# Performance work log

Measured on AMD Instinct MI355X. Metric: run time of the kernel, lower is better.

The kernel has to match this reference:

```python
import jax, jax.numpy as jnp
import numpy as np

N, C, T, V = 16, 128, 150, 25
NH, DK, DV = 8, 32, 128          # dk = 0.25*128, dv = out_channels
DKH, DVH = DK // NH, DV // NH    # 4, 16
EPS = 1e-5


def setup_inputs() -> dict:
    key = jax.random.key(0)
    ks = jax.random.split(key, 14)
    qkv_out = 2 * DK + DV  # 192
    return {
        "x": jax.random.normal(ks[0], (N, C, T, V), jnp.float32),
        "qkv_w": jax.random.normal(ks[1], (qkv_out, C), jnp.float32) * (1.0 / np.sqrt(C)),
        "qkv_b": jax.random.normal(ks[2], (qkv_out,), jnp.float32) * 0.01,
        "key_rel": jax.random.normal(ks[3], (2 * T - 1, DKH), jnp.float32),
        "attn_w": jax.random.normal(ks[4], (DV, DV), jnp.float32) * (1.0 / np.sqrt(DV)),
        "attn_b": jax.random.normal(ks[5], (DV,), jnp.float32) * 0.01,
        "dbn_g": jnp.ones((C * V,), jnp.float32),
        "dbn_b": jnp.zeros((C * V,), jnp.float32),
        "dbn_m": jax.random.normal(ks[6], (C * V,), jnp.float32) * 0.01,
        "dbn_v": jax.random.uniform(ks[7], (C * V,), jnp.float32, 0.5, 1.5),
        "bn_g": jnp.ones((DV,), jnp.float32),
        "bn_b": jnp.zeros((DV,), jnp.float32),
        "bn_m": jax.random.normal(ks[8], (DV,), jnp.float32) * 0.01,
        "bn_v": jax.random.uniform(ks[9], (DV,), jnp.float32, 0.5, 1.5),
    }


def rel_to_abs(x):
    # x: [B, H, L, 2L-1] relative logits -> [B, H, L, L] absolute logits
    B, H, L, _ = x.shape
    x = jnp.pad(x, ((0, 0), (0, 0), (0, 0), (0, 1)))          # [B,H,L,2L]
    flat = x.reshape(B, H, L * 2 * L)
    flat = jnp.pad(flat, ((0, 0), (0, 0), (0, L - 1)))
    return flat.reshape(B, H, L + 1, 2 * L - 1)[:, :, :L, L - 1:]


def reference(x, qkv_w, qkv_b, key_rel, attn_w, attn_b,
              dbn_g, dbn_b, dbn_m, dbn_v, bn_g, bn_b, bn_m, bn_v):
    n, c, t, v = x.shape
    x_sum = x
    # data_bn (BatchNorm1d over C*V channels, inference mode)
    xn = x.transpose(0, 1, 3, 2).reshape(n, c * v, t)
    xn = (xn - dbn_m[None, :, None]) * (dbn_g / jnp.sqrt(dbn_v + EPS))[None, :, None] + dbn_b[None, :, None]
    xn = xn.reshape(n, c, v, t).transpose(0, 1, 3, 2)
    # fold nodes into batch: [N,C,T,V] -> [N*V, C, T]
    xb = xn.transpose(0, 3, 1, 2).reshape(n * v, c, t)
    # pointwise qkv conv (kernel 1x1)
    qkv = jnp.einsum('bct,oc->bot', xb, qkv_w) + qkv_b[None, :, None]
    q = qkv[:, :DK]
    k = qkv[:, DK:2 * DK]
    val = qkv[:, 2 * DK:]
    B = n * v
    q = q.reshape(B, NH, DKH, t) * (DKH ** -0.5)   # scaled before rel logits, as in torch
    k = k.reshape(B, NH, DKH, t)
    val = val.reshape(B, NH, DVH, t)
    logits = jnp.einsum('bhdt,bhds->bhts', q, k)    # [B,NH,T,T]
    rel = jnp.einsum('bhdt,md->bhtm', q, key_rel)   # [B,NH,T,2T-1]
    logits = logits + rel_to_abs(rel)
    weights = jax.nn.softmax(logits, axis=-1)
    out = jnp.einsum('bhts,bhds->bhtd', weights, val)  # [B,NH,T,DVH]
    # combine heads -> [B, DV, T], then 1x1 attn_out conv
    out = out.transpose(0, 1, 3, 2).reshape(B, DV, t)
    out = jnp.einsum('bct,oc->bot', out, attn_w) + attn_b[None, :, None]
    # unfold nodes: [N*V, DV, T] -> [N, DV, T, V]
    out = out.reshape(n, v, DV, t).transpose(0, 2, 3, 1)
    res = out + x_sum
    # BatchNorm2d over channel dim (inference mode)
    res = (res - bn_m[None, :, None, None]) * (bn_g / jnp.sqrt(bn_v + EPS))[None, :, None, None] + bn_b[None, :, None, None]
    return jax.nn.relu(res)
```

## Files before the change

### kernel.cpp

```cpp
#include <hip/hip_runtime.h>
#include <math.h>

#define N_   16
#define C_   128
#define T_   150
#define V_   25
#define NH_  8
#define DK_  32
#define DV_  128
#define B_   400
#define QO_  192
#define EPS_ 1e-5f

typedef __attribute__((ext_vector_type(4))) short bf16x4;
typedef __attribute__((ext_vector_type(4))) float f32x4;
typedef __attribute__((ext_vector_type(8))) short short8;

__device__ inline f32x4 mfma16(bf16x4 a, bf16x4 b, f32x4 c) {
#if __has_builtin(__builtin_amdgcn_mfma_f32_16x16x16bf16_1k)
  return __builtin_amdgcn_mfma_f32_16x16x16bf16_1k(a, b, c, 0, 0, 0);
#else
  asm volatile("v_mfma_f32_16x16x16_bf16 %0, %1, %2, %0"
               : "+v"(c) : "v"(a), "v"(b));
  return c;
#endif
}

__device__ inline short f2bf(float f) {
  union { float f; unsigned u; } v; v.f = f;
  unsigned u = v.u + 0x7fffu + ((v.u >> 16) & 1u);
  return (short)(u >> 16);
}
__device__ inline float lo16(unsigned u) { union { unsigned u; float f; } v; v.u = u << 16;        return v.f; }
__device__ inline float hi16(unsigned u) { union { unsigned u; float f; } v; v.u = u & 0xffff0000u; return v.f; }
__device__ inline unsigned pk2(float a, float b) {
  union { float f; unsigned u; } x, y; x.f = a; y.f = b;
  return ((x.u + 0x8000u) >> 16) | ((y.u + 0x8000u) & 0xffff0000u);
}
__device__ inline unsigned pktr(float a, float b) {
  union { float f; unsigned u; } x, y; x.f = a; y.f = b;
#if __has_builtin(__builtin_amdgcn_perm)
  return __builtin_amdgcn_perm(y.u, x.u, 0x07060302u);
#else
  return (x.u >> 16) | (y.u & 0xffff0000u);
#endif
}

__global__ __launch_bounds__(256) void k_prep(
    const float* __restrict__ qkv_w, const float* __restrict__ attn_w,
    const float* __restrict__ dbn_g, const float* __restrict__ dbn_b,
    const float* __restrict__ dbn_m, const float* __restrict__ dbn_v,
    const float* __restrict__ key_rel,
    short* __restrict__ wqb, short* __restrict__ wab,
    short* __restrict__ krbg,
    float* __restrict__ dsc, float* __restrict__ dsh)
{
  const int tid = blockIdx.x*256 + threadIdx.x;
  const int nthr = gridDim.x*256;
  for (int i = tid; i < QO_*C_; i += nthr) wqb[i] = f2bf(qkv_w[i]);
  for (int i = tid; i < DV_*DV_; i += nthr) wab[i] = f2bf(attn_w[i]);
  for (int i = tid; i < 336*4; i += nthr) {
    int m = (i >> 2) - 16;
    krbg[i] = (m >= 0 && m < 2*T_-1) ? f2bf(key_rel[m*4 + (i & 3)]) : (short)0;
  }
  for (int i = tid; i < C_*V_; i += nthr) {
    float sc = dbn_g[i] * rsqrtf(dbn_v[i] + EPS_);
    dsc[i] = sc;
    dsh[i] = dbn_b[i] - dbn_m[i]*sc;
  }
}

__global__ __launch_bounds__(256) void k_xt2(
    const float* __restrict__ x, const float* __restrict__ dsc,
    const float* __restrict__ dsh, short* __restrict__ xtb)
{
  const int n = blockIdx.x, tv0 = blockIdx.y * 125;
  __shared__ short ls[C_][126];
  for (int i = threadIdx.x; i < C_*125; i += 256) {
    int c = i / 125, j = i % 125;
    int cv = c*V_ + j % 25;
    ls[c][j] = f2bf(x[((size_t)n*C_ + c)*(T_*V_) + tv0 + j] * dsc[cv] + dsh[cv]);
  }
  __syncthreads();
  for (int i = threadIdx.x; i < 125*C_; i += 256) {
    int j = i >> 7, c = i & 127;
    int tv = tv0 + j, t = tv / 25, v = tv % 25;
    xtb[((size_t)(n*V_ + v)*T_ + t)*C_ + c] = ls[c][j];
  }
}

__global__ __launch_bounds__(256) void k_qkv(
    const short* __restrict__ xtb, const short* __restrict__ wqb,
    const float* __restrict__ qkv_b, short* __restrict__ qkvb)
{
  const int b = blockIdx.x, t0 = blockIdx.y * 80;
  __shared__ short xs[80][136];
  for (int i = threadIdx.x; i < 80*16; i += 256) {
    int tt = i >> 4, ch = i & 15, t = t0 + tt;
    short8 vv = {0,0,0,0,0,0,0,0};
    if (t < T_) vv = *(const short8*)&xtb[((size_t)b*T_ + t)*C_ + ch*8];
    *(short8*)&xs[tt][ch*8] = vv;
  }
  __syncthreads();
  const int wave = threadIdx.x >> 6, lane = threadIdx.x & 63;
  const int tl = lane & 15, g = lane >> 4;
  const int ob = wave * 48;

  bf16x4 afr[3][8];
  #pragma unroll
  for (int mt = 0; mt < 3; ++mt)
    #pragma unroll
    for (int ks = 0; ks < 8; ++ks)
      afr[mt][ks] = *(const bf16x4*)&wqb[(ob + mt*16 + tl)*C_ + ks*16 + g*4];

  const f32x4 zero = {0.f,0.f,0.f,0.f};
  f32x4 acc[3][5];
  #pragma unroll
  for (int mt = 0; mt < 3; ++mt)
    #pragma unroll
    for (int nt = 0; nt < 5; ++nt) acc[mt][nt] = zero;

  #pragma unroll
  for (int ks = 0; ks < 8; ++ks) {
    bf16x4 bfr[5];
    #pragma unroll
    for (int nt = 0; nt < 5; ++nt)
      bfr[nt] = *(const bf16x4*)&xs[nt*16 + tl][ks*16 + g*4];
    #pragma unroll
    for (int mt = 0; mt < 3; ++mt)
      #pragma unroll
      for (int nt = 0; nt < 5; ++nt)
        acc[mt][nt] = mfma16(afr[mt][ks], bfr[nt], acc[mt][nt]);
  }

  float bia[3][4], scm[3];
  #pragma unroll
  for (int mt = 0; mt < 3; ++mt) {
    scm[mt] = (ob + mt*16 < DK_) ? (0.5f*1.44269504f) : 1.f;
    #pragma unroll
    for (int r = 0; r < 4; ++r) bia[mt][r] = qkv_b[ob + mt*16 + g*4 + r];
  }

  #pragma unroll
  for (int nt = 0; nt < 5; ++nt) {
    int tg = t0 + nt*16 + tl;
    if (tg >= T_) continue;
    #pragma unroll
    for (int mt = 0; mt < 3; ++mt) {
      int o = ob + mt*16 + g*4;
      short* dst = &qkvb[((size_t)b*QO_ + o)*T_ + tg];
      #pragma unroll
      for (int r = 0; r < 4; ++r)
        dst[r*T_] = f2bf((acc[mt][nt][r] + bia[mt][r]) * scm[mt]);
    }
  }
}

__global__ __launch_bounds__(256) void k_attn(
    const short* __restrict__ qkvb, const short* __restrict__ krbg,
    short* __restrict__ o2b)
{
  const int bh = blockIdx.x;
  const int b  = bh >> 3, h = bh & 7;
  __shared__ short kbc[160*4];
  __shared__ short qbc[160*4];
  __shared__ short ve[16][164];
  __shared__ short krb[336*4];
  const short* base = qkvb + (size_t)b*QO_*T_;
  const int tid = threadIdx.x;

  for (int i = tid; i < 320; i += 256) {
    int d = i / 80, j = i % 80, s = 2*j;
    unsigned u = 0;
    if (j < 75) u = *(const unsigned*)&base[(DK_ + h*4 + d)*T_ + s];
    kbc[s*4 + d] = (short)u;
    kbc[(s+1)*4 + d] = (short)(u >> 16);
  }
  for (int i = tid; i < 320; i += 256) {
    int d = i / 80, j = i % 80, t = 2*j;
    unsigned u = 0;
    if (j < 75) u = *(const unsigned*)&base[(h*4 + d)*T_ + t];
    qbc[t*4 + d] = (short)u;
    qbc[(t+1)*4 + d] = (short)(u >> 16);
  }
  for (int i = tid; i < 1280; i += 256) {
    int e = i / 80, j = i % 80;
    unsigned u = 0;
    if (j < 75) u = *(const unsigned*)&base[(2*DK_ + h*16 + e)*T_ + 2*j];
    *(unsigned*)&ve[e][2*j] = u;
  }
  for (int i = tid; i < 672; i += 256)
    *(unsigned*)&krb[2*i] = *(const unsigned*)&krbg[2*i];
  __syncthreads();

  const int wave = tid >> 6, lane = tid & 63;
  const int tl = lane & 15, g = lane >> 4, soff = g << 2;

  const bf16x4 zerob = {0, 0, 0, 0};
  const f32x4 zero = {0.f, 0.f, 0.f, 0.f};

  bf16x4 kfr[10], vfr[10];
  #pragma unroll
  for (int st = 0; st < 10; ++st) {
    kfr[st] = (g == 0) ? *(const bf16x4*)&kbc[(st*16 + tl)*4] : zerob;
    vfr[st] = *(const bf16x4*)&ve[tl][st*16 + soff];
  }

  const bool act = (g == (tl & 3));
  const int kca = tl >> 2;

  for (int tt = wave; tt < 10; tt += 4) {
    const int t0 = tt*16, tg = t0 + tl;
    union { unsigned u[2]; bf16x4 v; } bqu;
    bqu.v = *(const bf16x4*)&qbc[tg*4];
    const bf16x4 qfr = (g == 0) ? bqu.v : zerob;

    f32x4 c[10];
    #pragma unroll
    for (int st = 0; st < 10; ++st) c[st] = mfma16(kfr[st], qfr, zero);

    bf16x4 brel[4];
    #pragma unroll
    for (int kc = 0; kc < 4; ++kc)
      brel[kc] = (act && kc == kca) ? bqu.v : zerob;

    const bf16x4* krp = ((const bf16x4*)krb) + (tl - g + 165 - t0);
    #pragma unroll
    for (int st = 0; st < 10; ++st)
      #pragma unroll
      for (int kc = 0; kc < 4; ++kc)
        c[st] = mfma16(krp[st*16 - kc*4], brel[kc], c[st]);

    #pragma unroll
    for (int i = 0; i < 4; ++i)
      if (soff + i >= 6) c[9][i] = -3.0e38f;

    float l = 0.f;
    f32x4 acc = zero;
    #pragma unroll
    for (int st = 0; st < 10; ++st) {
      float p0 = __builtin_exp2f(c[st][0]);
      float p1 = __builtin_exp2f(c[st][1]);
      float p2 = __builtin_exp2f(c[st][2]);
      float p3 = __builtin_exp2f(c[st][3]);
      l += (p0 + p1) + (p2 + p3);
      union { unsigned u[2]; bf16x4 v; } pf;
      pf.u[0] = pktr(p0, p1); pf.u[1] = pktr(p2, p3);
      acc = mfma16(vfr[st], pf.v, acc);
    }
    l += __shfl_xor(l, 16);
    l += __shfl_xor(l, 32);
    const float inv = __builtin_amdgcn_rcpf(l);

    if (tg < T_) {
      unsigned u0 = pk2(acc[0]*inv, acc[1]*inv);
      unsigned u1 = pk2(acc[2]*inv, acc[3]*inv);
      *(uint2*)&o2b[((size_t)b*T_ + tg)*DV_ + h*16 + soff] = make_uint2(u0, u1);
    }
  }
}

__global__ __launch_bounds__(256) void k_proj(
    const short* __restrict__ o2b, const short* __restrict__ wab,
    const float* __restrict__ attn_b, short* __restrict__ projb)
{
  const int b = blockIdx.x, t0 = blockIdx.y * 80;
  __shared__ short xs[80][136];
  for (int i = threadIdx.x; i < 80*16; i += 256) {
    int tt = i >> 4, ch = i & 15, t = t0 + tt;
    short8 vv = {0,0,0,0,0,0,0,0};
    if (t < T_) vv = *(const short8*)&o2b[((size_t)b*T_ + t)*DV_ + ch*8];
    *(short8*)&xs[tt][ch*8] = vv;
  }
  __syncthreads();
  const int wave = threadIdx.x >> 6, lane = threadIdx.x & 63;
  const int tl = lane & 15, g = lane >> 4;
  const int ob = wave * 32;

  bf16x4 afr[2][8];
  #pragma unroll
  for (int mt = 0; mt < 2; ++mt)
    #pragma unroll
    for (int ks = 0; ks < 8; ++ks)
      afr[mt][ks] = *(const bf16x4*)&wab[(ob + mt*16 + tl)*DV_ + ks*16 + g*4];

  const f32x4 zero = {0.f,0.f,0.f,0.f};
  f32x4 acc[2][5];
  #pragma unroll
  for (int mt = 0; mt < 2; ++mt)
    #pragma unroll
    for (int nt = 0; nt < 5; ++nt) acc[mt][nt] = zero;

  #pragma unroll
  for (int ks = 0; ks < 8; ++ks) {
    bf16x4 bfr[5];
    #pragma unroll
    for (int nt = 0; nt < 5; ++nt)
      bfr[nt] = *(const bf16x4*)&xs[nt*16 + tl][ks*16 + g*4];
    #pragma unroll
    for (int mt = 0; mt < 2; ++mt)
      #pragma unroll
      for (int nt = 0; nt < 5; ++nt)
        acc[mt][nt] = mfma16(afr[mt][ks], bfr[nt], acc[mt][nt]);
  }

  float bia[2][4];
  #pragma unroll
  for (int mt = 0; mt < 2; ++mt)
    #pragma unroll
    for (int r = 0; r < 4; ++r) bia[mt][r] = attn_b[ob + mt*16 + g*4 + r];

  #pragma unroll
  for (int nt = 0; nt < 5; ++nt) {
    int tg = t0 + nt*16 + tl;
    if (tg >= T_) continue;
    #pragma unroll
    for (int mt = 0; mt < 2; ++mt) {
      int o = ob + mt*16 + g*4;
      short* dst = &projb[((size_t)b*DV_ + o)*T_ + tg];
      #pragma unroll
      for (int r = 0; r < 4; ++r)
        dst[r*T_] = f2bf(acc[mt][nt][r] + bia[mt][r]);
    }
  }
}

__global__ __launch_bounds__(256) void k_final(
    const short* __restrict__ projb, const float* __restrict__ x,
    const float* __restrict__ bn_g, const float* __restrict__ bn_b,
    const float* __restrict__ bn_m, const float* __restrict__ bn_v,
    float* __restrict__ out)
{
  const int n = blockIdx.x, o = blockIdx.y;
  __shared__ short ls[V_*T_];
  for (int i = threadIdx.x; i < V_*T_; i += 256) {
    int v = i / T_, t = i % T_;
    ls[i] = projb[((size_t)(n*V_ + v)*DV_ + o)*T_ + t];
  }
  __syncthreads();
  const float sc = bn_g[o] * rsqrtf(bn_v[o] + EPS_);
  const float sh = bn_b[o] - bn_m[o]*sc;
  const size_t base = ((size_t)n*C_ + o)*(T_*V_);
  for (int j = threadIdx.x; j < T_*V_; j += 256) {
    int t = j / V_, v = j % V_;
    float pv = lo16((unsigned)(unsigned short)ls[v*T_ + t]);
    float r = (pv + x[base + j]) * sc + sh;
    out[base + j] = fmaxf(r, 0.f);
  }
}

extern "C" void kernel_launch(void* const* d_in, const int* in_sizes, int n_in,
                              void* d_out, int out_size, void* d_ws, size_t ws_size,
                              hipStream_t stream) {
  const float* x       = (const float*)d_in[0];
  const float* qkv_w   = (const float*)d_in[1];
  const float* qkv_b   = (const float*)d_in[2];
  const float* key_rel = (const float*)d_in[3];
  const float* attn_w  = (const float*)d_in[4];
  const float* attn_b  = (const float*)d_in[5];
  const float* dbn_g   = (const float*)d_in[6];
  const float* dbn_b   = (const float*)d_in[7];
  const float* dbn_m   = (const float*)d_in[8];
  const float* dbn_v   = (const float*)d_in[9];
  const float* bn_g    = (const float*)d_in[10];
  const float* bn_b    = (const float*)d_in[11];
  const float* bn_m    = (const float*)d_in[12];
  const float* bn_v    = (const float*)d_in[13];

  short* xtb  = (short*)d_ws;
  short* o2b  = xtb;
  short* qkvb = xtb + (size_t)B_*C_*T_;
  float* projf = (float*)(qkvb + (size_t)B_*QO_*T_);
  short* projb = (short*)projf;
  float* dsc  = projf + (size_t)B_*DV_*T_;
  float* dsh  = dsc + C_*V_;
  short* wqb  = (short*)(dsh + C_*V_);
  short* wab  = wqb + QO_*C_;
  short* krbg = wab + DV_*DV_;
  float* outp = (float*)d_out;

  k_prep<<<32, 256, 0, stream>>>(qkv_w, attn_w, dbn_g, dbn_b, dbn_m, dbn_v,
                                 key_rel, wqb, wab, krbg, dsc, dsh);
  k_xt2<<<dim3(N_, 30), 256, 0, stream>>>(x, dsc, dsh, xtb);
  k_qkv<<<dim3(B_, 2), 256, 0, stream>>>(xtb, wqb, qkv_b, qkvb);
  k_attn<<<dim3(B_*NH_), 256, 0, stream>>>(qkvb, krbg, o2b);
  k_proj<<<dim3(B_, 2), 256, 0, stream>>>(o2b, wab, attn_b, projb);
  k_final<<<dim3(N_, DV_), 256, 0, stream>>>(projb, x, bn_g, bn_b, bn_m, bn_v, outp);
}
```

Before: 127.2 us.

## Process two attention heads per block in k_attn to balance wave work

Each attention block now handles two heads of the same batch element instead of one, so 20 row tiles are spread over 4 waves (5 each) rather than 10 tiles over 4 waves with two waves idle for the last round. The shared relative-key table load is amortized over two heads and the grid is halved. In exchange each block uses roughly twice the LDS for K/Q/V, and K/V fragments are reloaded when a wave switches heads, which may reduce occupancy.

```diff
diff --git a/kernel.cpp b/kernel.cpp
--- a/kernel.cpp
+++ b/kernel.cpp
@@ -161,33 +161,36 @@
     short* __restrict__ o2b)
 {
   const int bh = blockIdx.x;
-  const int b  = bh >> 3, h = bh & 7;
-  __shared__ short kbc[160*4];
-  __shared__ short qbc[160*4];
-  __shared__ short ve[16][164];
+  const int b  = bh >> 2, h0 = (bh & 3) * 2;
+  __shared__ short kbc[2][160*4];
+  __shared__ short qbc[2][160*4];
+  __shared__ short ve[2][16][164];
   __shared__ short krb[336*4];
   const short* base = qkvb + (size_t)b*QO_*T_;
   const int tid = threadIdx.x;
 
-  for (int i = tid; i < 320; i += 256) {
-    int d = i / 80, j = i % 80, s = 2*j;
+  for (int i = tid; i < 640; i += 256) {
+    int hh = i / 320, r = i - hh*320;
+    int d = r / 80, j = r - d*80, s = 2*j;
     unsigned u = 0;
-    if (j < 75) u = *(const unsigned*)&base[(DK_ + h*4 + d)*T_ + s];
-    kbc[s*4 + d] = (short)u;
-    kbc[(s+1)*4 + d] = (short)(u >> 16);
-  }
-  for (int i = tid; i < 320; i += 256) {
-    int d = i / 80, j = i % 80, t = 2*j;
+    if (j < 75) u = *(const unsigned*)&base[(DK_ + (h0+hh)*4 + d)*T_ + s];
+    kbc[hh][s*4 + d] = (short)u;
+    kbc[hh][(s+1)*4 + d] = (short)(u >> 16);
+  }
+  for (int i = tid; i < 640; i += 256) {
+    int hh = i / 320, r = i - hh*320;
+    int d = r / 80, j = r - d*80, t = 2*j;
     unsigned u = 0;
-    if (j < 75) u = *(const unsigned*)&base[(h*4 + d)*T_ + t];
-    qbc[t*4 + d] = (short)u;
-    qbc[(t+1)*4 + d] = (short)(u >> 16);
-  }
-  for (int i = tid; i < 1280; i += 256) {
-    int e = i / 80, j = i % 80;
+    if (j < 75) u = *(const unsigned*)&base[((h0+hh)*4 + d)*T_ + t];
+    qbc[hh][t*4 + d] = (short)u;
+    qbc[hh][(t+1)*4 + d] = (short)(u >> 16);
+  }
+  for (int i = tid; i < 2560; i += 256) {
+    int hh = i / 1280, r = i - hh*1280;
+    int e = r / 80, j = r - e*80;
     unsigned u = 0;
-    if (j < 75) u = *(const unsigned*)&base[(2*DK_ + h*16 + e)*T_ + 2*j];
-    *(unsigned*)&ve[e][2*j] = u;
+    if (j < 75) u = *(const unsigned*)&base[(2*DK_ + (h0+hh)*16 + e)*T_ + 2*j];
+    *(unsigned*)&ve[hh][e][2*j] = u;
   }
   for (int i = tid; i < 672; i += 256)
     *(unsigned*)&krb[2*i] = *(const unsigned*)&krbg[2*i];
@@ -199,20 +202,27 @@
   const bf16x4 zerob = {0, 0, 0, 0};
   const f32x4 zero = {0.f, 0.f, 0.f, 0.f};
 
-  bf16x4 kfr[10], vfr[10];
-  #pragma unroll
-  for (int st = 0; st < 10; ++st) {
-    kfr[st] = (g == 0) ? *(const bf16x4*)&kbc[(st*16 + tl)*4] : zerob;
-    vfr[st] = *(const bf16x4*)&ve[tl][st*16 + soff];
-  }
-
   const bool act = (g == (tl & 3));
   const int kca = tl >> 2;
 
-  for (int tt = wave; tt < 10; tt += 4) {
+  bf16x4 kfr[10], vfr[10];
+  int hh_cur = -1;
+
+  for (int u = wave; u < 20; u += 4) {
+    const int hh = (u >= 10) ? 1 : 0;
+    const int tt = u - hh*10;
+    if (hh != hh_cur) {
+      #pragma unroll
+      for (int st = 0; st < 10; ++st) {
+        kfr[st] = (g == 0) ? *(const bf16x4*)&kbc[hh][(st*16 + tl)*4] : zerob;
+        vfr[st] = *(const bf16x4*)&ve[hh][tl][st*16 + soff];
+      }
+      hh_cur = hh;
+    }
+
     const int t0 = tt*16, tg = t0 + tl;
     union { unsigned u[2]; bf16x4 v; } bqu;
-    bqu.v = *(const bf16x4*)&qbc[tg*4];
+    bqu.v = *(const bf16x4*)&qbc[hh][tg*4];
     const bf16x4 qfr = (g == 0) ? bqu.v : zerob;
 
     f32x4 c[10];
@@ -255,7 +265,7 @@
     if (tg < T_) {
       unsigned u0 = pk2(acc[0]*inv, acc[1]*inv);
       unsigned u1 = pk2(acc[2]*inv, acc[3]*inv);
-      *(uint2*)&o2b[((size_t)b*T_ + tg)*DV_ + h*16 + soff] = make_uint2(u0, u1);
+      *(uint2*)&o2b[((size_t)b*T_ + tg)*DV_ + (h0+hh)*16 + soff] = make_uint2(u0, u1);
     }
   }
 }
@@ -383,7 +393,7 @@
                                  key_rel, wqb, wab, krbg, dsc, dsh);
   k_xt2<<<dim3(N_, 30), 256, 0, stream>>>(x, dsc, dsh, xtb);
   k_qkv<<<dim3(B_, 2), 256, 0, stream>>>(xtb, wqb, qkv_b, qkvb);
-  k_attn<<<dim3(B_*NH_), 256, 0, stream>>>(qkvb, krbg, o2b);
+  k_attn<<<dim3(B_*NH_/2), 256, 0, stream>>>(qkvb, krbg, o2b);
   k_proj<<<dim3(B_, 2), 256, 0, stream>>>(o2b, wab, attn_b, projb);
   k_final<<<dim3(N_, DV_), 256, 0, stream>>>(projb, x, bn_g, bn_b, bn_m, bn_v, outp);
 }
```

Result: slower. 137.1 us (+7.8%).
